# Kernel tuning notes

Hardware: AMD Instinct MI355X
Metric: run time of the kernel (lower is better)

Reference implementation:

```python
import jax, jax.numpy as jnp
import numpy as np

B, D, P, F = 128, 18, 64, 1024
H = 16            # nhead
HD = F // H       # head dim = 64
NUM_CLASSES = 23
MLP_HID = 4 * F
EPS = 1e-5


def ln(x, g, b):
    m = jnp.mean(x, axis=-1, keepdims=True)
    v = jnp.mean((x - m) ** 2, axis=-1, keepdims=True)
    return (x - m) * jax.lax.rsqrt(v + EPS) * g + b


def setup_inputs() -> dict:
    key = jax.random.key(0)
    ks = jax.random.split(key, 20)
    s = 0.02
    inp = {
        "x": jax.random.normal(ks[0], (B, D, P, F), dtype=jnp.float32),
        "channel_query": jax.random.normal(ks[1], (1, 1, F), dtype=jnp.float32),
        "cls_query": jax.random.normal(ks[2], (1, 1, F), dtype=jnp.float32),
        # MHA params, stored (in, out) layout
        "ch_in_w": jax.random.normal(ks[3], (F, 3 * F), dtype=jnp.float32) * s,
        "ch_in_b": jnp.zeros((3 * F,), jnp.float32),
        "ch_out_w": jax.random.normal(ks[4], (F, F), dtype=jnp.float32) * s,
        "ch_out_b": jnp.zeros((F,), jnp.float32),
        "t_in_w": jax.random.normal(ks[5], (F, 3 * F), dtype=jnp.float32) * s,
        "t_in_b": jnp.zeros((3 * F,), jnp.float32),
        "t_out_w": jax.random.normal(ks[6], (F, F), dtype=jnp.float32) * s,
        "t_out_b": jnp.zeros((F,), jnp.float32),
        # LayerNorm params
        "qn_g": jnp.ones((F,), jnp.float32), "qn_b": jnp.zeros((F,), jnp.float32),
        "cn_g": jnp.ones((F,), jnp.float32), "cn_b": jnp.zeros((F,), jnp.float32),
        "pnc_g": jnp.ones((F,), jnp.float32), "pnc_b": jnp.zeros((F,), jnp.float32),
        "pnp_g": jnp.ones((F,), jnp.float32), "pnp_b": jnp.zeros((F,), jnp.float32),
        "pon_g": jnp.ones((F,), jnp.float32), "pon_b": jnp.zeros((F,), jnp.float32),
        # classifier MLP
        "w1": jax.random.normal(ks[7], (F, MLP_HID), dtype=jnp.float32) * s,
        "b1": jnp.zeros((MLP_HID,), jnp.float32),
        "w2": jax.random.normal(ks[8], (MLP_HID, NUM_CLASSES), dtype=jnp.float32) * s,
        "b2": jnp.zeros((NUM_CLASSES,), jnp.float32),
    }
    return inp


def _forward(x, channel_query, cls_query, ch_in_w, ch_in_b, ch_out_w, ch_out_b,
             t_in_w, t_in_b, t_out_w, t_out_b, qn_g, qn_b, cn_g, cn_b,
             pnc_g, pnc_b, pnp_g, pnp_b, pon_g, pon_b, w1, b1, w2, b2):
    scale = 1.0 / jnp.sqrt(jnp.float32(HD))

    # ---- Stage 1: per-patch cross-channel attention pooling ----
    q = ln(channel_query, qn_g, qn_b)[0, 0]                 # (F,) shared query
    qh = (q @ ch_in_w[:, :F] + ch_in_b[:F]).reshape(H, HD)  # (H, HD)
    tokens = x.transpose(0, 2, 1, 3)                        # (B, P, D, F)
    kp = (tokens @ ch_in_w[:, F:2 * F] + ch_in_b[F:2 * F]).reshape(B, P, D, H, HD)
    vp = (tokens @ ch_in_w[:, 2 * F:] + ch_in_b[2 * F:]).reshape(B, P, D, H, HD)
    scores = jnp.einsum('hd,bpkhd->bphk', qh, kp) * scale   # (B, P, H, D)
    attn = jax.nn.softmax(scores, axis=-1)
    pooled = jnp.einsum('bphk,bpkhd->bphd', attn, vp).reshape(B, P, F)
    pooled = pooled @ ch_out_w + ch_out_b
    fused = ln(pooled, cn_g, cn_b)                          # (B, P, F)

    # ---- Stage 2: temporal attention pooling (query len 1 vs P keys) ----
    cq = ln(cls_query, pnc_g, pnc_b)[0, 0]                  # (F,)
    kv = ln(fused, pnp_g, pnp_b)                            # (B, P, F)
    qh2 = (cq @ t_in_w[:, :F] + t_in_b[:F]).reshape(H, HD)
    kp2 = (kv @ t_in_w[:, F:2 * F] + t_in_b[F:2 * F]).reshape(B, P, H, HD)
    vp2 = (kv @ t_in_w[:, 2 * F:] + t_in_b[2 * F:]).reshape(B, P, H, HD)
    scores2 = jnp.einsum('hd,bkhd->bhk', qh2, kp2) * scale  # (B, H, P)
    attn2 = jax.nn.softmax(scores2, axis=-1)
    pooled2 = jnp.einsum('bhk,bkhd->bhd', attn2, vp2).reshape(B, F)
    pooled2 = pooled2 @ t_out_w + t_out_b
    pooled2 = ln(pooled2, pon_g, pon_b)                     # (B, F)

    # ---- Stage 3: MLP classifier (dropout off in eval) ----
    h = jax.nn.gelu(pooled2 @ w1 + b1, approximate=False)
    logits = h @ w2 + b2                                    # (B, num_classes)
    return logits


def reference(x, channel_query, cls_query, ch_in_w, ch_in_b, ch_out_w, ch_out_b,
              t_in_w, t_in_b, t_out_w, t_out_b, qn_g, qn_b, cn_g, cn_b,
              pnc_g, pnc_b, pnp_g, pnp_b, pon_g, pon_b, w1, b1, w2, b2):
    return _forward(x, channel_query, cls_query, ch_in_w, ch_in_b, ch_out_w, ch_out_b,
                    t_in_w, t_in_b, t_out_w, t_out_b, qn_g, qn_b, cn_g, cn_b,
                    pnc_g, pnc_b, pnp_g, pnp_b, pon_g, pon_b, w1, b1, w2, b2)
```

## Files before the change

kernel.cpp:

```cpp
#include <hip/hip_runtime.h>
#include <stdint.h>

typedef __attribute__((ext_vector_type(4))) float  fx4;
typedef __attribute__((ext_vector_type(8))) short  bs8;

union Frag8 { bs8 s; unsigned u[4]; };

__device__ __forceinline__ unsigned short f2b(float f){
  union { float f; unsigned u; } v; v.f = f;
  unsigned r = (v.u + 0x7FFFu + ((v.u >> 16) & 1u)) >> 16;
  return (unsigned short)r;
}
__device__ __forceinline__ float b2f(unsigned short s){
  union { unsigned u; float f; } v; v.u = ((unsigned)s) << 16;
  return v.f;
}
__device__ __forceinline__ unsigned pack2(float a, float b){
  return (unsigned)f2b(a) | ((unsigned)f2b(b) << 16);
}

__device__ __forceinline__ float blk_sum(float v, float* scr, int t){
#pragma unroll
  for (int i = 1; i < 64; i <<= 1) v += __shfl_xor(v, i, 64);
  __syncthreads();
  if ((t & 63) == 0) scr[t >> 6] = v;
  __syncthreads();
  return scr[0] + scr[1] + scr[2] + scr[3];
}

__global__ __launch_bounds__(256) void k_lnvec(
    const float* in0, const float* g0, const float* b0, float* out0,
    const float* in1, const float* g1, const float* b1, float* out1)
{
  __shared__ float scr[4];
  const float* in = blockIdx.x ? in1 : in0;
  const float* g  = blockIdx.x ? g1  : g0;
  const float* bb = blockIdx.x ? b1  : b0;
  float* out      = blockIdx.x ? out1 : out0;
  int t = threadIdx.x;
  float4 v = *(const float4*)(in + t*4);
  float s = blk_sum(v.x+v.y+v.z+v.w, scr, t);
  float mean = s * (1.0f/1024.0f);
  float4 d; d.x=v.x-mean; d.y=v.y-mean; d.z=v.z-mean; d.w=v.w-mean;
  float ss = blk_sum(d.x*d.x+d.y*d.y+d.z*d.z+d.w*d.w, scr, t);
  float rs = rsqrtf(ss*(1.0f/1024.0f) + 1e-5f);
  float4 gv = *(const float4*)(g + t*4);
  float4 bv = *(const float4*)(bb + t*4);
  float4 o; o.x=d.x*rs*gv.x+bv.x; o.y=d.y*rs*gv.y+bv.y; o.z=d.z*rs*gv.z+bv.z; o.w=d.w*rs*gv.w+bv.w;
  *(float4*)(out + t*4) = o;
}

__global__ __launch_bounds__(256) void k_gemv(
    const float* q0, const float* W0, const float* bias0, float* out0,
    const float* q1, const float* W1, const float* bias1, float* out1)
{
  int blk = blockIdx.x;
  int sel = blk >= 32;
  const float* qv = sel ? q1 : q0;
  const float* W  = sel ? W1 : W0;
  const float* bi = sel ? bias1 : bias0;
  float* ov       = sel ? out1 : out0;
  int j0 = (blk & 31) * 32;
  int t = threadIdx.x;
  int jl = t >> 3, l8 = t & 7;
  int j = j0 + jl;
  const float* Wc = W + j;
  float s = 0.f;
  for (int i = 0; i < 128; i++){
    int f = l8*128 + i;
    s += qv[f] * Wc[(long)f*3072];
  }
  s += __shfl_xor(s, 1, 64); s += __shfl_xor(s, 2, 64); s += __shfl_xor(s, 4, 64);
  if (l8 == 0) ov[j] = s + bi[j];
}

__global__ __launch_bounds__(256) void k_weff(
    const float* qh0, const float* W0, const float* bv0, unsigned short* outB0, float* ce0,
    const float* qh1, const float* W1, const float* bv1, unsigned short* outB1, float* ce1)
{
  int blk = blockIdx.x; int sel = blk >= 64; int fb = blk & 63;
  const float* qs = sel ? qh1 : qh0;
  const float* W  = sel ? W1  : W0;
  const float* bv = sel ? bv1 : bv0;
  unsigned short* oB = sel ? outB1 : outB0;
  float* ce = sel ? ce1 : ce0;
  int t = threadIdx.x; int h = t & 15, fl = t >> 4;
  int f = fb*16 + fl;
  const float* Wr = W + (long)f*3072 + 1024 + h*64;
  const float* qr = qs + h*64;
  float s = 0.f;
#pragma unroll 8
  for (int d = 0; d < 64; d++) s += Wr[d]*qr[d];
  int idx = (f>>5)*512 + ((f>>3)&3)*128 + h*8 + (f&7);
  oB[idx] = f2b(s);
  if (fb == 0 && t < 16){
    float c = 0.f;
    for (int d = 0; d < 64; d++) c += bv[1024 + t*64 + d]*qs[t*64+d];
    ce[t] = c;
  }
}

__global__ __launch_bounds__(256) void k_transpose(
    const float* inA, long strA, unsigned short* outA, int cntA,
    const float* inB, long strB, unsigned short* outB, int cntB,
    const float* inC, long strC, unsigned short* outC, int cntC,
    const float* inD, long strD, unsigned short* outD, int cntD,
    const float* inE, long strE, unsigned short* outE, int cntE)
{
  int id = blockIdx.x;
  const float* in; long str; unsigned short* out;
  if (id < cntA){ in=inA; str=strA; out=outA; }
  else { id -= cntA;
    if (id < cntB){ in=inB; str=strB; out=outB; }
    else { id -= cntB;
      if (id < cntC){ in=inC; str=strC; out=outC; }
      else { id -= cntC;
        if (id < cntD){ in=inD; str=strD; out=outD; }
        else { id -= cntD; in=inE; str=strE; out=outE; }
      }
    }
  }
  int kt = id & 31, nt = id >> 5;
  __shared__ __align__(16) unsigned short tile[32][33];
  int t = threadIdx.x;
  int r = t >> 3, c4 = (t & 7)*4;
  float4 v = *(const float4*)(in + (long)(kt*32 + r)*str + nt*32 + c4);
  tile[c4+0][r] = f2b(v.x); tile[c4+1][r] = f2b(v.y);
  tile[c4+2][r] = f2b(v.z); tile[c4+3][r] = f2b(v.w);
  __syncthreads();
  int n = t >> 3, k4 = (t & 7)*4;
  ushort4 o; o.x = tile[n][k4]; o.y = tile[n][k4+1]; o.z = tile[n][k4+2]; o.w = tile[n][k4+3];
  *(ushort4*)(out + (long)(nt*32 + n)*1024 + kt*32 + k4) = o;
}

__global__ __launch_bounds__(256) void k1_attn(
    const float* __restrict__ x,
    const unsigned short* __restrict__ weffB, const float* __restrict__ ceff,
    unsigned short* __restrict__ ctx, int bp0)
{
  __shared__ __align__(16) unsigned short tok[18*1032];
  __shared__ float S[18*16];
  __shared__ float attn[18*16];
  int bp = bp0 + blockIdx.x;
  int b = bp >> 6, p = bp & 63;
  int t = threadIdx.x;
  int w = t >> 6, l = t & 63, q = l >> 4, l16 = l & 15;

  if (w < 2){
    int mlog = w*16 + l16;
    int m = mlog > 17 ? 17 : mlog;
    const float* xrow = x + (((long)b*18 + m)*64 + p)*1024;
    bool store = (w == 0) || (l16 < 2);
    fx4 acc = {0.f,0.f,0.f,0.f};
#pragma unroll 4
    for (int kk = 0; kk < 32; kk++){
      int f0 = kk*32 + q*8;
      float4 a0 = *(const float4*)(xrow + f0);
      float4 a1 = *(const float4*)(xrow + f0 + 4);
      Frag8 af;
      af.u[0] = pack2(a0.x,a0.y); af.u[1] = pack2(a0.z,a0.w);
      af.u[2] = pack2(a1.x,a1.y); af.u[3] = pack2(a1.z,a1.w);
      bs8 bf = *(const bs8*)(weffB + (kk*64 + l)*8);
      acc = __builtin_amdgcn_mfma_f32_16x16x32_bf16(af.s, bf, acc, 0, 0, 0);
      if (store) *(bs8*)(&tok[m*1032 + f0]) = af.s;
    }
    float cf = ceff[l16];
#pragma unroll
    for (int i = 0; i < 4; i++){
      int r = w*16 + q*4 + i;
      if (r < 18) S[r*16 + l16] = (acc[i] + cf) * 0.125f;
    }
  }
  __syncthreads();
  if (t < 16){
    float mx = -1e30f;
    for (int k = 0; k < 18; k++) mx = fmaxf(mx, S[k*16+t]);
    float e[18]; float sm = 0.f;
    for (int k = 0; k < 18; k++){ e[k] = expf(S[k*16+t]-mx); sm += e[k]; }
    float inv = 1.f/sm;
    for (int k = 0; k < 18; k++) attn[k*16+t] = e[k]*inv;
  }
  __syncthreads();

  float4 a4[16];
#pragma unroll
  for (int h = 0; h < 16; h++){ a4[h].x=0.f; a4[h].y=0.f; a4[h].z=0.f; a4[h].w=0.f; }
  for (int k = 0; k < 18; k++){
    ushort4 t4 = *(const ushort4*)(&tok[k*1032 + t*4]);
    float x0=b2f(t4.x), x1=b2f(t4.y), x2=b2f(t4.z), x3=b2f(t4.w);
#pragma unroll
    for (int h = 0; h < 16; h++){
      float a = attn[k*16+h];
      a4[h].x += a*x0; a4[h].y += a*x1; a4[h].z += a*x2; a4[h].w += a*x3;
    }
  }
  unsigned short* crow = ctx + ((long)blockIdx.x*16)*1024 + t*4;
#pragma unroll
  for (int h = 0; h < 16; h++){
    uint2 o = make_uint2(pack2(a4[h].x, a4[h].y), pack2(a4[h].z, a4[h].w));
    *(uint2*)(crow + (long)h*1024) = o;
  }
}

__global__ __launch_bounds__(256) void k_gemm(
    const unsigned short* __restrict__ A, long strideA, long colAstep,
    const unsigned short* __restrict__ BT, int Kfull,
    const float* __restrict__ bias,
    void* __restrict__ Cout, long strideC, int outBf16, int doGelu, int K)
{
  __shared__ __align__(16) unsigned short As[128*72];
  __shared__ __align__(16) unsigned short Bs[64*72];
  int t = threadIdx.x;
  int w = t >> 6, l = t & 63, q = l >> 4, l16 = l & 15;
  long mbase = (long)blockIdx.x * 128;
  int nb = blockIdx.y;
  const unsigned short* Ab = A + mbase*strideA + (long)nb*colAstep;
  const unsigned short* Bb = BT + (long)nb*64*Kfull;
  fx4 acc[2][4];
#pragma unroll
  for (int mf = 0; mf < 2; mf++)
#pragma unroll
    for (int nf = 0; nf < 4; nf++) acc[mf][nf] = (fx4){0.f,0.f,0.f,0.f};

  int ar = t >> 1, ac = (t & 1)*32;
  int bn = t >> 2, bc = (t & 3)*16;

  for (int k0 = 0; k0 < K; k0 += 64){
    const unsigned short* asrc = Ab + (long)ar*strideA + k0 + ac;
    uint4 av0 = *(const uint4*)(asrc);
    uint4 av1 = *(const uint4*)(asrc + 8);
    uint4 av2 = *(const uint4*)(asrc + 16);
    uint4 av3 = *(const uint4*)(asrc + 24);
    const unsigned short* bsrc = Bb + (long)bn*Kfull + k0 + bc;
    uint4 bv0 = *(const uint4*)(bsrc);
    uint4 bv1 = *(const uint4*)(bsrc + 8);
    __syncthreads();
    *(uint4*)(&As[ar*72 + ac +  0]) = av0;
    *(uint4*)(&As[ar*72 + ac +  8]) = av1;
    *(uint4*)(&As[ar*72 + ac + 16]) = av2;
    *(uint4*)(&As[ar*72 + ac + 24]) = av3;
    *(uint4*)(&Bs[bn*72 + bc + 0]) = bv0;
    *(uint4*)(&Bs[bn*72 + bc + 8]) = bv1;
    __syncthreads();
#pragma unroll
    for (int ks = 0; ks < 64; ks += 32){
      bs8 a0 = *(const bs8*)(&As[(w*32 +      l16)*72 + ks + q*8]);
      bs8 a1 = *(const bs8*)(&As[(w*32 + 16 + l16)*72 + ks + q*8]);
#pragma unroll
      for (int nf = 0; nf < 4; nf++){
        bs8 bf = *(const bs8*)(&Bs[(nf*16 + l16)*72 + ks + q*8]);
        acc[0][nf] = __builtin_amdgcn_mfma_f32_16x16x32_bf16(a0, bf, acc[0][nf], 0,0,0);
        acc[1][nf] = __builtin_amdgcn_mfma_f32_16x16x32_bf16(a1, bf, acc[1][nf], 0,0,0);
      }
    }
  }
  float bv[4];
#pragma unroll
  for (int nf = 0; nf < 4; nf++) bv[nf] = bias[nb*64 + nf*16 + l16];
#pragma unroll
  for (int mf = 0; mf < 2; mf++)
#pragma unroll
    for (int nf = 0; nf < 4; nf++)
#pragma unroll
      for (int i = 0; i < 4; i++){
        long row = mbase + w*32 + mf*16 + q*4 + i;
        long col = (long)nb*64 + nf*16 + l16;
        float v = acc[mf][nf][i] + bv[nf];
        if (doGelu) v = 0.5f*v*(1.f + erff(v*0.70710678118654752f));
        if (outBf16) ((unsigned short*)Cout)[row*strideC + col] = f2b(v);
        else         ((float*)Cout)[row*strideC + col] = v;
      }
}

__global__ __launch_bounds__(256) void k_ln(
    const float* __restrict__ in,
    const float* __restrict__ g1, const float* __restrict__ b1,
    const float* __restrict__ g2, const float* __restrict__ b2, int two,
    unsigned short* __restrict__ out)
{
  __shared__ float scr[4];
  long row = blockIdx.x;
  int t = threadIdx.x;
  float4 v = *(const float4*)(in + row*1024 + t*4);
  float s = blk_sum(v.x+v.y+v.z+v.w, scr, t);
  float mean = s*(1.f/1024.f);
  float4 d; d.x=v.x-mean; d.y=v.y-mean; d.z=v.z-mean; d.w=v.w-mean;
  float ss = blk_sum(d.x*d.x+d.y*d.y+d.z*d.z+d.w*d.w, scr, t);
  float rs = rsqrtf(ss*(1.f/1024.f)+1e-5f);
  float4 g = *(const float4*)(g1+t*4); float4 bb = *(const float4*)(b1+t*4);
  float4 y; y.x=d.x*rs*g.x+bb.x; y.y=d.y*rs*g.y+bb.y; y.z=d.z*rs*g.z+bb.z; y.w=d.w*rs*g.w+bb.w;
  if (two){
    float s2 = blk_sum(y.x+y.y+y.z+y.w, scr, t);
    float m2 = s2*(1.f/1024.f);
    d.x=y.x-m2; d.y=y.y-m2; d.z=y.z-m2; d.w=y.w-m2;
    float ss2 = blk_sum(d.x*d.x+d.y*d.y+d.z*d.z+d.w*d.w, scr, t);
    float rs2 = rsqrtf(ss2*(1.f/1024.f)+1e-5f);
    g = *(const float4*)(g2+t*4); bb = *(const float4*)(b2+t*4);
    y.x=d.x*rs2*g.x+bb.x; y.y=d.y*rs2*g.y+bb.y; y.z=d.z*rs2*g.z+bb.z; y.w=d.w*rs2*g.w+bb.w;
  }
  uint2 o = make_uint2(pack2(y.x,y.y), pack2(y.z,y.w));
  *(uint2*)(out + row*1024 + t*4) = o;
}

__global__ __launch_bounds__(256) void k5_temporal(
    const unsigned short* __restrict__ kv,
    const unsigned short* __restrict__ weff2B, const float* __restrict__ ceff2,
    unsigned short* __restrict__ ctx2)
{
  __shared__ float S2[64*16];
  __shared__ float at2[64*16];
  int b = blockIdx.x;
  int t = threadIdx.x, w = t>>6, l = t&63, q = l>>4, l16 = l&15;
  const unsigned short* kvb = kv + (long)b*64*1024;
  {
    int p = w*16 + l16;
    const unsigned short* krow = kvb + (long)p*1024;
    fx4 acc = {0.f,0.f,0.f,0.f};
#pragma unroll 4
    for (int kk = 0; kk < 32; kk++){
      bs8 af = *(const bs8*)(krow + kk*32 + q*8);
      bs8 bf = *(const bs8*)(weff2B + (kk*64 + l)*8);
      acc = __builtin_amdgcn_mfma_f32_16x16x32_bf16(af, bf, acc, 0, 0, 0);
    }
    float cf = ceff2[l16];
#pragma unroll
    for (int i = 0; i < 4; i++) S2[(w*16 + q*4 + i)*16 + l16] = (acc[i]+cf)*0.125f;
  }
  __syncthreads();
  if (t < 16){
    float mx = -1e30f;
    for (int k = 0; k < 64; k++) mx = fmaxf(mx, S2[k*16+t]);
    float sm = 0.f;
    for (int k = 0; k < 64; k++){ float e = expf(S2[k*16+t]-mx); at2[k*16+t] = e; sm += e; }
    float inv = 1.f/sm;
    for (int k = 0; k < 64; k++) at2[k*16+t] *= inv;
  }
  __syncthreads();
  float4 a4[16];
#pragma unroll
  for (int h = 0; h < 16; h++){ a4[h].x=0.f; a4[h].y=0.f; a4[h].z=0.f; a4[h].w=0.f; }
  for (int p2 = 0; p2 < 64; p2++){
    ushort4 t4 = *(const ushort4*)(kvb + (long)p2*1024 + t*4);
    float x0=b2f(t4.x), x1=b2f(t4.y), x2=b2f(t4.z), x3=b2f(t4.w);
#pragma unroll
    for (int h = 0; h < 16; h++){
      float a = at2[p2*16+h];
      a4[h].x += a*x0; a4[h].y += a*x1; a4[h].z += a*x2; a4[h].w += a*x3;
    }
  }
  unsigned short* crow = ctx2 + ((long)b*16)*1024 + t*4;
#pragma unroll
  for (int h = 0; h < 16; h++){
    uint2 o = make_uint2(pack2(a4[h].x, a4[h].y), pack2(a4[h].z, a4[h].w));
    *(uint2*)(crow + (long)h*1024) = o;
  }
}

__global__ __launch_bounds__(256) void k9_logits(
    const unsigned short* __restrict__ h1,
    const float* __restrict__ w2, const float* __restrict__ b2, float* __restrict__ out)
{
  __shared__ __align__(16) unsigned short hrow[4096];
  int b = blockIdx.x, t = threadIdx.x;
  *(uint4*)(&hrow[t*16])     = *(const uint4*)(h1 + (long)b*4096 + t*16);
  *(uint4*)(&hrow[t*16 + 8]) = *(const uint4*)(h1 + (long)b*4096 + t*16 + 8);
  __syncthreads();
  int c = t >> 3, l8 = t & 7;
  if (c < 23){
    float s = 0.f;
    for (int i = 0; i < 512; i++){
      int f = l8*512 + i;
      s += b2f(hrow[f]) * w2[(long)f*23 + c];
    }
    s += __shfl_xor(s, 1, 64); s += __shfl_xor(s, 2, 64); s += __shfl_xor(s, 4, 64);
    if (l8 == 0) out[b*23 + c] = s + b2[c];
  }
}

extern "C" void kernel_launch(void* const* d_in, const int* in_sizes, int n_in,
                              void* d_out, int out_size, void* d_ws, size_t ws_size,
                              hipStream_t stream)
{
  const float* x        = (const float*)d_in[0];
  const float* chq      = (const float*)d_in[1];
  const float* clq      = (const float*)d_in[2];
  const float* ch_in_w  = (const float*)d_in[3];
  const float* ch_in_b  = (const float*)d_in[4];
  const float* ch_out_w = (const float*)d_in[5];
  const float* ch_out_b = (const float*)d_in[6];
  const float* t_in_w   = (const float*)d_in[7];
  const float* t_in_b   = (const float*)d_in[8];
  const float* t_out_w  = (const float*)d_in[9];
  const float* t_out_b  = (const float*)d_in[10];
  const float* qn_g  = (const float*)d_in[11]; const float* qn_b  = (const float*)d_in[12];
  const float* cn_g  = (const float*)d_in[13]; const float* cn_b  = (const float*)d_in[14];
  const float* pnc_g = (const float*)d_in[15]; const float* pnc_b = (const float*)d_in[16];
  const float* pnp_g = (const float*)d_in[17]; const float* pnp_b = (const float*)d_in[18];
  const float* pon_g = (const float*)d_in[19]; const float* pon_b = (const float*)d_in[20];
  const float* w1 = (const float*)d_in[21]; const float* b1 = (const float*)d_in[22];
  const float* w2 = (const float*)d_in[23]; const float* b2 = (const float*)d_in[24];
  float* out = (float*)d_out;

  char* ws = (char*)d_ws;
  size_t off = 0;
  auto alloc = [&](size_t bytes)->char*{
    char* p = ws + off; off += (bytes + 255) & ~(size_t)255; return p;
  };
  float* q_f   = (float*)alloc(4096);
  float* cq_f  = (float*)alloc(4096);
  float* qh_f  = (float*)alloc(4096);
  float* qh2_f = (float*)alloc(4096);
  float* ceff  = (float*)alloc(256);
  float* ceff2 = (float*)alloc(256);
  unsigned short* weffB  = (unsigned short*)alloc(32768);
  unsigned short* weff2B = (unsigned short*)alloc(32768);
  unsigned short* WvT   = (unsigned short*)alloc(2097152);
  unsigned short* WoutT = (unsigned short*)alloc(2097152);
  unsigned short* Wv2T  = (unsigned short*)alloc(2097152);
  unsigned short* toutT = (unsigned short*)alloc(2097152);
  unsigned short* w1T   = (unsigned short*)alloc(8388608);
  unsigned short* pooled   = (unsigned short*)alloc((size_t)8192*1024*2);
  float*          fusedpre = (float*)alloc((size_t)8192*1024*4);
  unsigned short* kvw      = (unsigned short*)alloc((size_t)8192*1024*2);
  unsigned short* ctx2     = (unsigned short*)alloc((size_t)128*16384*2);
  unsigned short* pooled2  = (unsigned short*)alloc((size_t)128*1024*2);
  float*          pre2     = (float*)alloc((size_t)128*1024*4);
  unsigned short* zbuf     = (unsigned short*)alloc((size_t)128*1024*2);
  unsigned short* h1buf    = (unsigned short*)alloc((size_t)128*4096*2);
  size_t base = off;
  size_t avail = ws_size > base ? ws_size - base : 0;
  long rows = (long)(avail / ((size_t)16*1024*2));
  if (rows > 8192) rows = 8192;
  rows &= ~127L;
  if (rows < 128) rows = 128;
  unsigned short* ctxbuf = (unsigned short*)(ws + base);

  k_lnvec<<<dim3(2), dim3(256), 0, stream>>>(chq, qn_g, qn_b, q_f, clq, pnc_g, pnc_b, cq_f);
  k_gemv<<<dim3(64), dim3(256), 0, stream>>>(q_f, ch_in_w, ch_in_b, qh_f, cq_f, t_in_w, t_in_b, qh2_f);
  k_weff<<<dim3(128), dim3(256), 0, stream>>>(qh_f, ch_in_w, ch_in_b, weffB, ceff,
                                              qh2_f, t_in_w, t_in_b, weff2B, ceff2);
  k_transpose<<<dim3(8192), dim3(256), 0, stream>>>(
      ch_in_w + 2048, (long)3072, WvT,   1024,
      ch_out_w,       (long)1024, WoutT, 1024,
      t_in_w + 2048,  (long)3072, Wv2T,  1024,
      t_out_w,        (long)1024, toutT, 1024,
      w1,             (long)4096, w1T,   4096);

  for (long bp0 = 0; bp0 < 8192; bp0 += rows){
    long cnt = (8192 - bp0 < rows) ? (8192 - bp0) : rows;
    k1_attn<<<dim3((unsigned)cnt), dim3(256), 0, stream>>>(x, weffB, ceff, ctxbuf, (int)bp0);
    k_gemm<<<dim3((unsigned)(cnt/128), 16), dim3(256), 0, stream>>>(
        ctxbuf, (long)16384, (long)1024, WvT, 1024, ch_in_b + 2048,
        (void*)(pooled + bp0*1024), (long)1024, 1, 0, 1024);
  }
  k_gemm<<<dim3(64,16), dim3(256), 0, stream>>>(
      pooled, (long)1024, (long)0, WoutT, 1024, ch_out_b,
      (void*)fusedpre, (long)1024, 0, 0, 1024);
  k_ln<<<dim3(8192), dim3(256), 0, stream>>>(fusedpre, cn_g, cn_b, pnp_g, pnp_b, 1, kvw);
  k5_temporal<<<dim3(128), dim3(256), 0, stream>>>(kvw, weff2B, ceff2, ctx2);
  k_gemm<<<dim3(1,16), dim3(256), 0, stream>>>(
      ctx2, (long)16384, (long)1024, Wv2T, 1024, t_in_b + 2048,
      (void*)pooled2, (long)1024, 1, 0, 1024);
  k_gemm<<<dim3(1,16), dim3(256), 0, stream>>>(
      pooled2, (long)1024, (long)0, toutT, 1024, t_out_b,
      (void*)pre2, (long)1024, 0, 0, 1024);
  k_ln<<<dim3(128), dim3(256), 0, stream>>>(pre2, pon_g, pon_b, pon_g, pon_b, 0, zbuf);
  k_gemm<<<dim3(1,64), dim3(256), 0, stream>>>(
      zbuf, (long)1024, (long)0, w1T, 1024, b1,
      (void*)h1buf, (long)4096, 1, 1, 1024);
  k9_logits<<<dim3(128), dim3(256), 0, stream>>>(h1buf, w2, b2, out);
}
```

Measured before the change: 1.257 ms.

## Split k1 score MFMA across all waves and compute context with MFMA

```diff
diff --git a/kernel.cpp b/kernel.cpp
--- a/kernel.cpp
+++ b/kernel.cpp
@@ -139,21 +139,24 @@
     unsigned short* __restrict__ ctx, int bp0)
 {
   __shared__ __align__(16) unsigned short tok[18*1032];
-  __shared__ float S[18*16];
+  __shared__ float Sp[2][18*16];
   __shared__ float attn[18*16];
   int bp = bp0 + blockIdx.x;
   int b = bp >> 6, p = bp & 63;
   int t = threadIdx.x;
   int w = t >> 6, l = t & 63, q = l >> 4, l16 = l & 15;
-
-  if (w < 2){
-    int mlog = w*16 + l16;
+  int half = w >> 1, wr = w & 1;
+
+  {
+    int mlog = wr*16 + l16;
     int m = mlog > 17 ? 17 : mlog;
     const float* xrow = x + (((long)b*18 + m)*64 + p)*1024;
-    bool store = (w == 0) || (l16 < 2);
+    bool store = (wr == 0) || (l16 < 2);
+    int msw = ((m >> 3) & 1) << 4;
     fx4 acc = {0.f,0.f,0.f,0.f};
+    int kk0 = half*16;
 #pragma unroll 4
-    for (int kk = 0; kk < 32; kk++){
+    for (int kk = kk0; kk < kk0+16; kk++){
       int f0 = kk*32 + q*8;
       float4 a0 = *(const float4*)(xrow + f0);
       float4 a1 = *(const float4*)(xrow + f0 + 4);
@@ -162,43 +165,66 @@
       af.u[2] = pack2(a1.x,a1.y); af.u[3] = pack2(a1.z,a1.w);
       bs8 bf = *(const bs8*)(weffB + (kk*64 + l)*8);
       acc = __builtin_amdgcn_mfma_f32_16x16x32_bf16(af.s, bf, acc, 0, 0, 0);
-      if (store) *(bs8*)(&tok[m*1032 + f0]) = af.s;
-    }
-    float cf = ceff[l16];
+      if (store) *(bs8*)(&tok[m*1032 + (f0 ^ msw)]) = af.s;
+    }
 #pragma unroll
     for (int i = 0; i < 4; i++){
-      int r = w*16 + q*4 + i;
-      if (r < 18) S[r*16 + l16] = (acc[i] + cf) * 0.125f;
+      int r = wr*16 + q*4 + i;
+      if (r < 18) Sp[half][r*16 + l16] = acc[i];
     }
   }
   __syncthreads();
   if (t < 16){
+    float cf = ceff[t];
+    float sv[18];
     float mx = -1e30f;
-    for (int k = 0; k < 18; k++) mx = fmaxf(mx, S[k*16+t]);
-    float e[18]; float sm = 0.f;
-    for (int k = 0; k < 18; k++){ e[k] = expf(S[k*16+t]-mx); sm += e[k]; }
+#pragma unroll
+    for (int k = 0; k < 18; k++){
+      float s = (Sp[0][k*16+t] + Sp[1][k*16+t] + cf) * 0.125f;
+      sv[k] = s; mx = fmaxf(mx, s);
+    }
+    float sm = 0.f;
+#pragma unroll
+    for (int k = 0; k < 18; k++){ float e = expf(sv[k]-mx); sv[k] = e; sm += e; }
     float inv = 1.f/sm;
-    for (int k = 0; k < 18; k++) attn[k*16+t] = e[k]*inv;
-  }
-  __syncthreads();
-
-  float4 a4[16];
-#pragma unroll
-  for (int h = 0; h < 16; h++){ a4[h].x=0.f; a4[h].y=0.f; a4[h].z=0.f; a4[h].w=0.f; }
-  for (int k = 0; k < 18; k++){
-    ushort4 t4 = *(const ushort4*)(&tok[k*1032 + t*4]);
-    float x0=b2f(t4.x), x1=b2f(t4.y), x2=b2f(t4.z), x3=b2f(t4.w);
-#pragma unroll
-    for (int h = 0; h < 16; h++){
-      float a = attn[k*16+h];
-      a4[h].x += a*x0; a4[h].y += a*x1; a4[h].z += a*x2; a4[h].w += a*x3;
-    }
-  }
-  unsigned short* crow = ctx + ((long)blockIdx.x*16)*1024 + t*4;
-#pragma unroll
-  for (int h = 0; h < 16; h++){
-    uint2 o = make_uint2(pack2(a4[h].x, a4[h].y), pack2(a4[h].z, a4[h].w));
-    *(uint2*)(crow + (long)h*1024) = o;
+#pragma unroll
+    for (int k = 0; k < 18; k++) attn[k*16+t] = sv[k]*inv;
+  }
+  __syncthreads();
+
+  Frag8 Bhi, Blo;
+#pragma unroll
+  for (int jj = 0; jj < 4; jj++){
+    int c0 = q*8 + jj*2, c1 = c0 + 1;
+    float a0 = (c0 < 18) ? attn[c0*16 + l16] : 0.f;
+    float a1 = (c1 < 18) ? attn[c1*16 + l16] : 0.f;
+    unsigned short h0 = f2b(a0), h1 = f2b(a1);
+    float r0 = a0 - b2f(h0), r1 = a1 - b2f(h1);
+    Bhi.u[jj] = (unsigned)h0 | ((unsigned)h1 << 16);
+    Blo.u[jj] = pack2(r0, r1);
+  }
+  unsigned short* crow = ctx + ((long)blockIdx.x*16 + l16)*1024 + q*4;
+  int Tbase = w*256;
+#pragma unroll 4
+  for (int tt = 0; tt < 16; tt++){
+    int Tb = Tbase + tt*16;
+    int fA = Tb + l16;
+    Frag8 A;
+#pragma unroll
+    for (int jj = 0; jj < 4; jj++){
+      int c0 = q*8 + jj*2, c1 = c0 + 1;
+      int c0c = c0 > 17 ? 17 : c0, c1c = c1 > 17 ? 17 : c1;
+      unsigned v0 = tok[c0c*1032 + (fA ^ (((c0c>>3)&1)<<4))];
+      unsigned v1 = tok[c1c*1032 + (fA ^ (((c1c>>3)&1)<<4))];
+      if (c0 > 17) v0 = 0;
+      if (c1 > 17) v1 = 0;
+      A.u[jj] = v0 | (v1 << 16);
+    }
+    fx4 acc = {0.f,0.f,0.f,0.f};
+    acc = __builtin_amdgcn_mfma_f32_16x16x32_bf16(A.s, Bhi.s, acc, 0, 0, 0);
+    acc = __builtin_amdgcn_mfma_f32_16x16x32_bf16(A.s, Blo.s, acc, 0, 0, 0);
+    uint2 o = make_uint2(pack2(acc[0],acc[1]), pack2(acc[2],acc[3]));
+    *(uint2*)(crow + Tb) = o;
   }
 }
 
@@ -430,7 +456,7 @@
   size_t base = off;
   size_t avail = ws_size > base ? ws_size - base : 0;
   long rows = (long)(avail / ((size_t)16*1024*2));
-  if (rows > 8192) rows = 8192;
+  if (rows > 2048) rows = 2048;
   rows &= ~127L;
   if (rows < 128) rows = 128;
   unsigned short* ctxbuf = (unsigned short*)(ws + base);
```

After: 1.224 ms (median of 2 runs). -2.6%, faster.
